# Performance work log

Hardware: AMD Instinct MI355X
Metric: run time of the kernel (lower is better)

## Reference

```python
import jax, jax.numpy as jnp
import numpy as np

N = 8192
D = 1024
TAU = 1.0
ALPHA = 1.0
BETA = 0.0


def setup_inputs() -> dict:
    key = jax.random.key(0)
    z = jax.random.normal(key, (2 * N, D), dtype=jnp.float32)
    return {"z": z}


def reference(z):
    n = z.shape[0] // 2
    x1, x2 = z[:n], z[n:]
    x1_abs = jnp.linalg.norm(x1, axis=1)  # [N]
    x2_abs = jnp.linalg.norm(x2, axis=1)  # [N]
    # cosine similarity matrix / tau: [N, N]
    matrix = jnp.einsum('ik,jk->ij', x1, x2) / (x1_abs[:, None] * x2_abs[None, :]) / TAU
    pos_sim = jnp.diagonal(matrix)                     # [N]
    neg_sim = (matrix.sum(axis=1) - pos_sim) / (n - 1)  # [N]
    sim_matrix = jnp.exp(matrix)
    pos = jnp.diagonal(sim_matrix)
    p_ij = pos / (sim_matrix.sum(axis=1) - pos)
    alpha = jax.lax.stop_gradient(p_ij - 1.0 + ALPHA)
    loss = -jnp.log(p_ij) - alpha * pos_sim + neg_sim * BETA
    return (loss.mean(), p_ij.mean())
```

## Files before the change

kernel.cpp:

```cpp
#include <hip/hip_runtime.h>
#include <hip/hip_bf16.h>

typedef __hip_bfloat16 bf16_t;
typedef __attribute__((ext_vector_type(8))) short  s16x8;
typedef __attribute__((ext_vector_type(4))) float  f32x4;

#define N_ROWS 8192
#define D_DIM  1024

#define GLOAD_LDS16(g, l)                                                     \
  __builtin_amdgcn_global_load_lds(                                           \
      (const __attribute__((address_space(1))) void*)(g),                     \
      (__attribute__((address_space(3))) void*)(l), 16, 0, 0)

#define WAITCNT_VM(n) asm volatile("s_waitcnt vmcnt(" #n ")" ::: "memory")

struct alignas(8) bf16x4_s { bf16_t x, y, z, w; };

__global__ void __launch_bounds__(256) normalize_kernel(
    const float* __restrict__ z, bf16_t* __restrict__ out,
    float* __restrict__ rowsum) {
  const int t = threadIdx.x;
  if (blockIdx.x < 32) rowsum[blockIdx.x * 256 + t] = 0.f;
  const int row  = blockIdx.x * 4 + (t >> 6);
  const int lane = t & 63;
  const float4* rp = (const float4*)(z + (size_t)row * D_DIM);
  float4 v[4];
#pragma unroll
  for (int j = 0; j < 4; ++j) v[j] = rp[lane + 64 * j];
  float ss = 0.f;
#pragma unroll
  for (int j = 0; j < 4; ++j)
    ss += v[j].x * v[j].x + v[j].y * v[j].y + v[j].z * v[j].z + v[j].w * v[j].w;
  ss += __shfl_xor(ss, 1);
  ss += __shfl_xor(ss, 2);
  ss += __shfl_xor(ss, 4);
  ss += __shfl_xor(ss, 8);
  ss += __shfl_xor(ss, 16);
  ss += __shfl_xor(ss, 32);
  const float rn = rsqrtf(ss);
  bf16x4_s* op = (bf16x4_s*)(out + (size_t)row * D_DIM);
#pragma unroll
  for (int j = 0; j < 4; ++j) {
    bf16x4_s o;
    o.x = __float2bfloat16(v[j].x * rn);
    o.y = __float2bfloat16(v[j].y * rn);
    o.z = __float2bfloat16(v[j].z * rn);
    o.w = __float2bfloat16(v[j].w * rn);
    op[lane + 64 * j] = o;
  }
}

__global__ void __launch_bounds__(512, 2) simexp_gemm(
    const bf16_t* __restrict__ A, const bf16_t* __restrict__ B,
    float* __restrict__ rowsum, float* __restrict__ pos_sim) {
  constexpr int BK   = 32;
  constexpr int ABUF = 256 * BK;
  constexpr int BUFE = 2 * ABUF;
  __shared__ bf16_t lds[4 * BUFE];

  const int t    = threadIdx.x;
  const int w    = t >> 6;
  const int lane = t & 63;
  const int wr   = w >> 2;
  const int wc   = w & 3;
  const int rb   = blockIdx.y, cb = blockIdx.x;
  const int row0 = rb * 256, col0 = cb * 256;

  const int srow = t >> 2;
  const int scol = (((t & 3) ^ ((t >> 3) & 3))) * 8;
  const size_t gA0 = (size_t)(row0 + srow) * D_DIM + scol;
  const size_t gA1 = gA0 + (size_t)128 * D_DIM;
  const size_t gB0 = (size_t)(col0 + srow) * D_DIM + scol;
  const size_t gB1 = gB0 + (size_t)128 * D_DIM;
  const int ldst = w * 512;

#define STAGE_A(dst, k0)                                        \
  do {                                                          \
    GLOAD_LDS16(A + gA0 + (k0), (dst) + ldst);                  \
    GLOAD_LDS16(A + gA1 + (k0), (dst) + 4096 + ldst);           \
  } while (0)
#define STAGE_B(dst, k0)                                        \
  do {                                                          \
    GLOAD_LDS16(B + gB0 + (k0), (dst) + ABUF + ldst);           \
    GLOAD_LDS16(B + gB1 + (k0), (dst) + ABUF + 4096 + ldst);    \
  } while (0)

  int offA[8], offB[4];
#pragma unroll
  for (int m = 0; m < 8; ++m) {
    const int r = wr * 128 + m * 16 + (lane & 15);
    offA[m] = r * 32 + (((lane >> 4) ^ ((r >> 1) & 3)) * 8);
  }
#pragma unroll
  for (int n = 0; n < 4; ++n) {
    const int r = wc * 64 + n * 16 + (lane & 15);
    offB[n] = r * 32 + (((lane >> 4) ^ ((r >> 1) & 3)) * 8);
  }

  f32x4 acc[8][4];
#pragma unroll
  for (int m = 0; m < 8; ++m)
#pragma unroll
    for (int n = 0; n < 4; ++n) acc[m][n] = (f32x4){0.f, 0.f, 0.f, 0.f};

  STAGE_A(lds, 0);                 STAGE_B(lds, 0);
  STAGE_A(lds + BUFE, BK);         STAGE_B(lds + BUFE, BK);
  STAGE_A(lds + 2 * BUFE, 2 * BK); STAGE_B(lds + 2 * BUFE, 2 * BK);
  WAITCNT_VM(8);
  __builtin_amdgcn_s_barrier();

#pragma unroll 1
  for (int kt = 0; kt < 32; ++kt) {
    const int k0n = (kt + 3) * BK;
    const bf16_t* Ab = lds + (kt & 3) * BUFE;
    const bf16_t* Bb = Ab + ABUF;
    bf16_t* nxt = lds + ((kt + 3) & 3) * BUFE;

    if (kt < 29) STAGE_A(nxt, k0n);
    s16x8 bf[4];
#pragma unroll
    for (int n = 0; n < 4; ++n) bf[n] = *(const s16x8*)&Bb[offB[n]];
    s16x8 af[4];
#pragma unroll
    for (int m = 0; m < 4; ++m) af[m] = *(const s16x8*)&Ab[offA[m]];
    __builtin_amdgcn_s_setprio(1);
#pragma unroll
    for (int m = 0; m < 4; ++m)
#pragma unroll
      for (int n = 0; n < 4; ++n)
        acc[m][n] = __builtin_amdgcn_mfma_f32_16x16x32_bf16(
            af[m], bf[n], acc[m][n], 0, 0, 0);
    __builtin_amdgcn_s_setprio(0);

    if (kt < 29) STAGE_B(nxt, k0n);
#pragma unroll
    for (int m = 0; m < 4; ++m) af[m] = *(const s16x8*)&Ab[offA[m + 4]];
    __builtin_amdgcn_s_setprio(1);
#pragma unroll
    for (int m = 0; m < 4; ++m)
#pragma unroll
      for (int n = 0; n < 4; ++n)
        acc[m + 4][n] = __builtin_amdgcn_mfma_f32_16x16x32_bf16(
            af[m], bf[n], acc[m + 4][n], 0, 0, 0);
    __builtin_amdgcn_s_setprio(0);

    if (kt < 29) {
      WAITCNT_VM(8);
      __builtin_amdgcn_s_barrier();
    } else if (kt == 29) {
      WAITCNT_VM(4);
      __builtin_amdgcn_s_barrier();
    } else if (kt == 30) {
      WAITCNT_VM(0);
      __builtin_amdgcn_s_barrier();
    }
  }

  if (rb == cb) {
#pragma unroll
    for (int m = 0; m < 8; ++m)
#pragma unroll
      for (int n = 0; n < 4; ++n)
#pragma unroll
        for (int r = 0; r < 4; ++r) {
          const int grow = wr * 128 + m * 16 + (lane >> 4) * 4 + r;
          const int gcol = wc * 64 + n * 16 + (lane & 15);
          if (grow == gcol) pos_sim[row0 + grow] = acc[m][n][r];
        }
  }

  __syncthreads();
  float* red = (float*)lds;
#pragma unroll
  for (int m = 0; m < 8; ++m)
#pragma unroll
    for (int r = 0; r < 4; ++r) {
      float s = 0.f;
#pragma unroll
      for (int n = 0; n < 4; ++n) s += __expf(acc[m][n][r]);
      s += __shfl_xor(s, 1);
      s += __shfl_xor(s, 2);
      s += __shfl_xor(s, 4);
      s += __shfl_xor(s, 8);
      if ((lane & 15) == 0) {
        const int row_local = wr * 128 + m * 16 + (lane >> 4) * 4 + r;
        red[wc * 256 + row_local] = s;
      }
    }
  __syncthreads();
  if (t < 256) {
    const float s4 = red[t] + red[256 + t] + red[512 + t] + red[768 + t];
    atomicAdd(&rowsum[row0 + t], s4);
  }
#undef STAGE_A
#undef STAGE_B
}

__global__ void __launch_bounds__(256) finalize_kernel(
    const float* __restrict__ rowsum, const float* __restrict__ pos_sim,
    float* __restrict__ out) {
  const int t = threadIdx.x;
  double lsum = 0.0, psum = 0.0;
  for (int i = t; i < N_ROWS; i += 256) {
    const float ps    = pos_sim[i];
    const float pos   = expf(ps);
    const float denom = rowsum[i] - pos;
    const float p     = pos / denom;
    lsum += (double)(-logf(p) - p * ps);
    psum += (double)p;
  }
  for (int off = 32; off; off >>= 1) {
    lsum += __shfl_down(lsum, off);
    psum += __shfl_down(psum, off);
  }
  __shared__ double sl[4], sp[4];
  const int wv = t >> 6, ln = t & 63;
  if (ln == 0) { sl[wv] = lsum; sp[wv] = psum; }
  __syncthreads();
  if (t == 0) {
    const double L = sl[0] + sl[1] + sl[2] + sl[3];
    const double P = sp[0] + sp[1] + sp[2] + sp[3];
    out[0] = (float)(L / N_ROWS);
    out[1] = (float)(P / N_ROWS);
  }
}

extern "C" void kernel_launch(void* const* d_in, const int* in_sizes, int n_in,
                              void* d_out, int out_size, void* d_ws,
                              size_t ws_size, hipStream_t stream) {
  const float* z = (const float*)d_in[0];
  float* out = (float*)d_out;

  char* ws = (char*)d_ws;
  bf16_t* AB = (bf16_t*)ws;
  float* rowsum  = (float*)(ws + (size_t)2 * N_ROWS * D_DIM * sizeof(bf16_t));
  float* pos_sim = rowsum + N_ROWS;

  normalize_kernel<<<2 * N_ROWS / 4, 256, 0, stream>>>(z, AB, rowsum);

  bf16_t* Amat = AB;
  bf16_t* Bmat = AB + (size_t)N_ROWS * D_DIM;
  dim3 grid(N_ROWS / 256, N_ROWS / 256);
  simexp_gemm<<<grid, 512, 0, stream>>>(Amat, Bmat, rowsum, pos_sim);

  finalize_kernel<<<1, 256, 0, stream>>>(rowsum, pos_sim, out);
}
```

Before: 246.4 us.

## Restructure GEMM main loop into two 64-wide K slots with finer-grained barriers

Measured after the change: 230.0 us. -6.7%, faster.

```diff
diff --git a/kernel.cpp b/kernel.cpp
--- a/kernel.cpp
+++ b/kernel.cpp
@@ -14,6 +14,12 @@
       (__attribute__((address_space(3))) void*)(l), 16, 0, 0)
 
 #define WAITCNT_VM(n) asm volatile("s_waitcnt vmcnt(" #n ")" ::: "memory")
+#define BARRIER_()                                                            \
+  do {                                                                        \
+    asm volatile("" ::: "memory");                                            \
+    __builtin_amdgcn_s_barrier();                                             \
+    asm volatile("" ::: "memory");                                            \
+  } while (0)
 
 struct alignas(8) bf16x4_s { bf16_t x, y, z, w; };
 
@@ -54,10 +60,8 @@
 __global__ void __launch_bounds__(512, 2) simexp_gemm(
     const bf16_t* __restrict__ A, const bf16_t* __restrict__ B,
     float* __restrict__ rowsum, float* __restrict__ pos_sim) {
-  constexpr int BK   = 32;
-  constexpr int ABUF = 256 * BK;
-  constexpr int BUFE = 2 * ABUF;
-  __shared__ bf16_t lds[4 * BUFE];
+  constexpr int SLOT = 32768;
+  __shared__ bf16_t lds[2 * SLOT];
 
   const int t    = threadIdx.x;
   const int w    = t >> 6;
@@ -68,22 +72,24 @@
   const int row0 = rb * 256, col0 = cb * 256;
 
   const int srow = t >> 2;
-  const int scol = (((t & 3) ^ ((t >> 3) & 3))) * 8;
-  const size_t gA0 = (size_t)(row0 + srow) * D_DIM + scol;
-  const size_t gA1 = gA0 + (size_t)128 * D_DIM;
-  const size_t gB0 = (size_t)(col0 + srow) * D_DIM + scol;
-  const size_t gB1 = gB0 + (size_t)128 * D_DIM;
+  const int scol = ((t & 3) ^ ((t >> 3) & 3)) * 8;
   const int ldst = w * 512;
 
-#define STAGE_A(dst, k0)                                        \
-  do {                                                          \
-    GLOAD_LDS16(A + gA0 + (k0), (dst) + ldst);                  \
-    GLOAD_LDS16(A + gA1 + (k0), (dst) + 4096 + ldst);           \
-  } while (0)
-#define STAGE_B(dst, k0)                                        \
-  do {                                                          \
-    GLOAD_LDS16(B + gB0 + (k0), (dst) + ABUF + ldst);           \
-    GLOAD_LDS16(B + gB1 + (k0), (dst) + ABUF + 4096 + ldst);    \
+#define STGA(s, kh, Tt)                                                       \
+  do {                                                                        \
+    const int gc = (Tt) * 64 + (kh) * 32 + scol;                              \
+    GLOAD_LDS16(A + (size_t)(row0 + srow) * D_DIM + gc,                       \
+                lds + (s) * SLOT + (kh) * 8192 + ldst);                       \
+    GLOAD_LDS16(A + (size_t)(row0 + 128 + srow) * D_DIM + gc,                 \
+                lds + (s) * SLOT + (kh) * 8192 + 4096 + ldst);                \
+  } while (0)
+#define STGB(s, kh, Tt)                                                       \
+  do {                                                                        \
+    const int gc = (Tt) * 64 + (kh) * 32 + scol;                              \
+    GLOAD_LDS16(B + (size_t)(col0 + srow) * D_DIM + gc,                       \
+                lds + (s) * SLOT + 16384 + (kh) * 8192 + ldst);               \
+    GLOAD_LDS16(B + (size_t)(col0 + 128 + srow) * D_DIM + gc,                 \
+                lds + (s) * SLOT + 16384 + (kh) * 8192 + 4096 + ldst);        \
   } while (0)
 
   int offA[8], offB[4];
@@ -104,58 +110,53 @@
 #pragma unroll
     for (int n = 0; n < 4; ++n) acc[m][n] = (f32x4){0.f, 0.f, 0.f, 0.f};
 
-  STAGE_A(lds, 0);                 STAGE_B(lds, 0);
-  STAGE_A(lds + BUFE, BK);         STAGE_B(lds + BUFE, BK);
-  STAGE_A(lds + 2 * BUFE, 2 * BK); STAGE_B(lds + 2 * BUFE, 2 * BK);
+#define LOADB4_(s, kh)                                                        \
+  do {                                                                        \
+    _Pragma("unroll") for (int n = 0; n < 4; ++n) bfv[n] =                    \
+        *(const s16x8*)&lds[(s) * SLOT + 16384 + (kh) * 8192 + offB[n]];      \
+  } while (0)
+#define LOADA4_(s, kh, mb)                                                    \
+  do {                                                                        \
+    _Pragma("unroll") for (int m = 0; m < 4; ++m) afv[m] =                    \
+        *(const s16x8*)&lds[(s) * SLOT + (kh) * 8192 + offA[(mb) + m]];       \
+  } while (0)
+#define MFMA16_(mb)                                                           \
+  do {                                                                        \
+    __builtin_amdgcn_s_setprio(1);                                            \
+    _Pragma("unroll") for (int m = 0; m < 4; ++m)                             \
+        _Pragma("unroll") for (int n = 0; n < 4; ++n) acc[(mb) + m][n] =      \
+            __builtin_amdgcn_mfma_f32_16x16x32_bf16(afv[m], bfv[n],           \
+                                                    acc[(mb) + m][n], 0, 0, 0); \
+    __builtin_amdgcn_s_setprio(0);                                            \
+  } while (0)
+
+#define KWIN(s, S1, S2, S3, S4, W2, W4)                                       \
+  do {                                                                        \
+    s16x8 bfv[4], afv[4];                                                     \
+    LOADB4_(s, 0); LOADA4_(s, 0, 0); S1; MFMA16_(0); BARRIER_();              \
+    LOADA4_(s, 0, 4); S2; MFMA16_(4); W2; BARRIER_();                         \
+    LOADB4_(s, 1); LOADA4_(s, 1, 0); S3; MFMA16_(0); BARRIER_();              \
+    LOADA4_(s, 1, 4); S4; MFMA16_(4); W4; BARRIER_();                         \
+  } while (0)
+
+  STGA(0, 0, 0); STGB(0, 0, 0);
+  STGA(0, 1, 0); STGB(0, 1, 0);
+  STGA(1, 0, 1); STGB(1, 0, 1);
   WAITCNT_VM(8);
-  __builtin_amdgcn_s_barrier();
+  BARRIER_();
 
 #pragma unroll 1
-  for (int kt = 0; kt < 32; ++kt) {
-    const int k0n = (kt + 3) * BK;
-    const bf16_t* Ab = lds + (kt & 3) * BUFE;
-    const bf16_t* Bb = Ab + ABUF;
-    bf16_t* nxt = lds + ((kt + 3) & 3) * BUFE;
-
-    if (kt < 29) STAGE_A(nxt, k0n);
-    s16x8 bf[4];
-#pragma unroll
-    for (int n = 0; n < 4; ++n) bf[n] = *(const s16x8*)&Bb[offB[n]];
-    s16x8 af[4];
-#pragma unroll
-    for (int m = 0; m < 4; ++m) af[m] = *(const s16x8*)&Ab[offA[m]];
-    __builtin_amdgcn_s_setprio(1);
-#pragma unroll
-    for (int m = 0; m < 4; ++m)
-#pragma unroll
-      for (int n = 0; n < 4; ++n)
-        acc[m][n] = __builtin_amdgcn_mfma_f32_16x16x32_bf16(
-            af[m], bf[n], acc[m][n], 0, 0, 0);
-    __builtin_amdgcn_s_setprio(0);
-
-    if (kt < 29) STAGE_B(nxt, k0n);
-#pragma unroll
-    for (int m = 0; m < 4; ++m) af[m] = *(const s16x8*)&Ab[offA[m + 4]];
-    __builtin_amdgcn_s_setprio(1);
-#pragma unroll
-    for (int m = 0; m < 4; ++m)
-#pragma unroll
-      for (int n = 0; n < 4; ++n)
-        acc[m + 4][n] = __builtin_amdgcn_mfma_f32_16x16x32_bf16(
-            af[m], bf[n], acc[m + 4][n], 0, 0, 0);
-    __builtin_amdgcn_s_setprio(0);
-
-    if (kt < 29) {
-      WAITCNT_VM(8);
-      __builtin_amdgcn_s_barrier();
-    } else if (kt == 29) {
-      WAITCNT_VM(4);
-      __builtin_amdgcn_s_barrier();
-    } else if (kt == 30) {
-      WAITCNT_VM(0);
-      __builtin_amdgcn_s_barrier();
-    }
-  }
+  for (int i = 0; i < 7; ++i) {
+    const int T = 2 * i;
+    KWIN(0, STGA(1, 1, T + 1), STGB(1, 1, T + 1),
+            STGA(0, 0, T + 2), STGB(0, 0, T + 2),
+            WAITCNT_VM(8), WAITCNT_VM(8));
+    KWIN(1, STGA(0, 1, T + 2), STGB(0, 1, T + 2),
+            STGA(1, 0, T + 3), STGB(1, 0, T + 3),
+            WAITCNT_VM(8), WAITCNT_VM(8));
+  }
+  KWIN(0, STGA(1, 1, 15), STGB(1, 1, 15), , , WAITCNT_VM(8), WAITCNT_VM(4));
+  KWIN(1, , , , , WAITCNT_VM(0), );
 
   if (rb == cb) {
 #pragma unroll
@@ -193,8 +194,12 @@
     const float s4 = red[t] + red[256 + t] + red[512 + t] + red[768 + t];
     atomicAdd(&rowsum[row0 + t], s4);
   }
-#undef STAGE_A
-#undef STAGE_B
+#undef STGA
+#undef STGB
+#undef LOADB4_
+#undef LOADA4_
+#undef MFMA16_
+#undef KWIN
 }
 
 __global__ void __launch_bounds__(256) finalize_kernel(
```
